# Optimization experiments

Measured on AMD Instinct MI355X. Metric: run time of the kernel, lower is better.

Reference implementation:

```python
import jax, jax.numpy as jnp
import numpy as np

N = 100000      # num nodes
E = 1600000     # num edges (avg degree 16)
D_IN = 64
D_OUT = 32
NEG_SLOPE = 0.01  # torch LeakyReLU default


def setup_inputs() -> dict:
    key = jax.random.key(0)
    k1, k2, k3, k4 = jax.random.split(key, 4)
    x = jax.random.normal(k1, (N, D_IN), dtype=jnp.float32)
    edge_index = jax.random.randint(k2, (2, E), 0, N, dtype=jnp.int32)
    # GCNConv linear weights (glorot-ish init) and biases
    W1 = jax.random.normal(k3, (D_IN, D_IN), dtype=jnp.float32) / np.float32(np.sqrt(D_IN))
    b1 = jnp.zeros((D_IN,), dtype=jnp.float32)
    W2 = jax.random.normal(k4, (D_IN, D_OUT), dtype=jnp.float32) / np.float32(np.sqrt(D_IN))
    b2 = jnp.zeros((D_OUT,), dtype=jnp.float32)
    return {"x": x, "edge_index": edge_index, "W1": W1, "b1": b1, "W2": W2, "b2": b2}


def reference(x, edge_index, W1, b1, W2, b2):
    # PyG GCNConv default: add self-loops, symmetric normalization D^-1/2 (A+I) D^-1/2
    loops = jnp.arange(N, dtype=edge_index.dtype)
    src = jnp.concatenate([edge_index[0], loops])  # [E+N]
    dst = jnp.concatenate([edge_index[1], loops])  # [E+N]
    deg = jax.ops.segment_sum(jnp.ones(src.shape[0], jnp.float32), dst, num_segments=N)
    dinv = jax.lax.rsqrt(deg)  # deg >= 1 due to self-loops
    norm = dinv[src] * dinv[dst]  # [E+N]

    def gcn_conv(h, W, b):
        h = h @ W                          # [N, d_out]
        msg = h[src] * norm[:, None]       # gather + normalize  [E+N, d_out]
        return jax.ops.segment_sum(msg, dst, num_segments=N) + b  # scatter-add

    h = gcn_conv(x, W1, b1)
    h = jnp.where(h > 0, h, NEG_SLOPE * h)  # LeakyReLU
    return gcn_conv(h, W2, b2)
```

## Files before the change

kernel.cpp:

```cpp
#include <hip/hip_runtime.h>

#define N_NODES 100000
#define N_EDGES 1600000
#define DIN 64
#define DOUT 32
#define NEG_SLOPE 0.01f
#define NBUCK 196
#define CAP 12288
#define CH 4096
#define NB1 ((N_EDGES + CH - 1) / CH)

__device__ inline unsigned short f2bf(float f) {
    unsigned int u = __float_as_uint(f);
    unsigned int r = (u + 0x7fffu + ((u >> 16) & 1u)) >> 16;
    return (unsigned short)r;
}
__device__ inline float bflo(unsigned int p) { return __uint_as_float(p << 16); }
__device__ inline float bfhi(unsigned int p) { return __uint_as_float(p & 0xffff0000u); }
#define NTL(p) __builtin_nontemporal_load(p)

__device__ inline void addpack4(float* a, uint4 r) {
    a[0] += bflo(r.x); a[1] += bfhi(r.x);
    a[2] += bflo(r.y); a[3] += bfhi(r.y);
    a[4] += bflo(r.z); a[5] += bfhi(r.z);
    a[6] += bflo(r.w); a[7] += bfhi(r.w);
}
__device__ inline void addpack2(float* a, uint2 r) {
    a[0] += bflo(r.x); a[1] += bfhi(r.x);
    a[2] += bflo(r.y); a[3] += bfhi(r.y);
}

__global__ __launch_bounds__(256) void binpass1_kernel(const int* __restrict__ src,
                                                       const int* __restrict__ dst,
                                                       int* __restrict__ bucketfill,
                                                       unsigned int* __restrict__ staging2) {
    __shared__ int histw[4][NBUCK];
    __shared__ int base[NBUCK];
    __shared__ int tot[NBUCK];
    __shared__ int gbase[NBUCK];
    __shared__ int scanbuf[256];
    __shared__ unsigned int sorted[CH];
    int tid = threadIdx.x;
    int w = tid >> 6;
    int b = blockIdx.x;
    for (int t = tid; t < 4 * NBUCK; t += 256) ((int*)histw)[t] = 0;
    __syncthreads();

    int e0 = b * CH + tid;
    int bk[16];
    int rk[16];
    unsigned int pay[16];
#pragma unroll
    for (int i = 0; i < 16; ++i) {
        int e = e0 + i * 256;
        if (e < N_EDGES) {
            int d = NTL(&dst[e]);
            int s = NTL(&src[e]);
            bk[i] = d >> 9;
            pay[i] = (unsigned int)s | ((unsigned int)(d & 511) << 17);
            rk[i] = atomicAdd(&histw[w][bk[i]], 1);
        } else {
            bk[i] = -1;
        }
    }
    __syncthreads();
    int v = 0;
    if (tid < NBUCK) {
        int h0 = histw[0][tid], h1 = histw[1][tid], h2 = histw[2][tid], h3 = histw[3][tid];
        histw[0][tid] = 0;
        histw[1][tid] = h0;
        histw[2][tid] = h0 + h1;
        histw[3][tid] = h0 + h1 + h2;
        v = h0 + h1 + h2 + h3;
        tot[tid] = v;
    }
    scanbuf[tid] = (tid < NBUCK) ? v : 0;
    __syncthreads();
    for (int off = 1; off < 256; off <<= 1) {
        int a = scanbuf[tid];
        int add = (tid >= off) ? scanbuf[tid - off] : 0;
        __syncthreads();
        scanbuf[tid] = a + add;
        __syncthreads();
    }
    if (tid < NBUCK) {
        base[tid] = scanbuf[tid] - v;
        gbase[tid] = v ? atomicAdd(&bucketfill[tid], v) : 0;
    }
    __syncthreads();
#pragma unroll
    for (int i = 0; i < 16; ++i) {
        if (bk[i] >= 0) sorted[base[bk[i]] + histw[w][bk[i]] + rk[i]] = pay[i];
    }
    __syncthreads();
    int wv = tid >> 6, ln = tid & 63;
    for (int k = wv; k < NBUCK; k += 4) {
        int h = tot[k];
        int b0 = base[k];
        int g0 = gbase[k];
        unsigned int* dp = staging2 + (size_t)k * CAP;
        for (int i = ln; i < h; i += 64)
            if (g0 + i < CAP) dp[g0 + i] = sorted[b0 + i];
    }
}

__global__ __launch_bounds__(1024) void binpass2_kernel(const unsigned int* __restrict__ staging2,
                                                        const int* __restrict__ bucketfill,
                                                        int* __restrict__ rowptr,
                                                        float* __restrict__ dinv,
                                                        int* __restrict__ colsrc) {
    __shared__ unsigned int coll[CAP];
    __shared__ int hist[512];
    __shared__ int posl[512];
    __shared__ int sh[512];
    __shared__ int red[4];
    int k = blockIdx.x;
    int tid = threadIdx.x;
    int base_node = k << 9;
    int nn = min(512, N_NODES - base_node);
    int len = min(bucketfill[k], CAP);

    if (tid < 256) {
        int v = (tid < k) ? bucketfill[tid] : 0;
#pragma unroll
        for (int off = 32; off; off >>= 1) v += __shfl_down(v, off);
        if ((tid & 63) == 0) red[tid >> 6] = v;
    }
    if (tid < 512) hist[tid] = 0;
    __syncthreads();
    int bbase = red[0] + red[1] + red[2] + red[3];
    const unsigned int* stg = staging2 + (size_t)k * CAP;

    for (int i = tid; i < len; i += 1024) coll[i] = NTL(&stg[i]);
    __syncthreads();
    for (int i = tid; i < len; i += 1024) atomicAdd(&hist[coll[i] >> 17], 1);
    __syncthreads();

    int v = 0;
    if (tid < 512) { v = hist[tid]; sh[tid] = v; }
    __syncthreads();
    for (int off = 1; off < 512; off <<= 1) {
        int a = 0, add = 0;
        if (tid < 512) { a = sh[tid]; add = (tid >= off) ? sh[tid - off] : 0; }
        __syncthreads();
        if (tid < 512) sh[tid] = a + add;
        __syncthreads();
    }
    if (tid < 512) {
        int excl = sh[tid] - v;
        posl[tid] = bbase + excl;
        if (tid < nn) {
            rowptr[base_node + tid] = bbase + excl;
            dinv[base_node + tid] = rsqrtf((float)(v + 1));
        }
    }
    if (k == NBUCK - 1 && tid == 0) rowptr[N_NODES] = N_EDGES;
    __syncthreads();
    for (int i = tid; i < len; i += 1024) {
        unsigned int pay = coll[i];
        int idx = atomicAdd(&posl[pay >> 17], 1);
        colsrc[idx] = (int)(pay & 0x1FFFFu);
    }
}

__global__ __launch_bounds__(256) void gemm_k64_n64_kernel(const float* __restrict__ X,
                                                           const float* __restrict__ W,
                                                           const float* __restrict__ dinv,
                                                           unsigned short* __restrict__ Hn) {
    __shared__ float Ws[64 * 64];
    __shared__ float Xs[64][65];
    int tid = threadIdx.x;
    int row0 = blockIdx.x * 64;
    {
        const float4* Wv = (const float4*)W;
        float4* Wsv = (float4*)Ws;
#pragma unroll
        for (int i = 0; i < 4; ++i) Wsv[tid + 256 * i] = Wv[tid + 256 * i];
    }
#pragma unroll
    for (int i = 0; i < 4; ++i) {
        int s = tid + i * 256;
        int r = s >> 4, c = (s & 15) * 4;
        int gr = row0 + r;
        float4 xv = (gr < N_NODES) ? *(const float4*)(X + (size_t)gr * 64 + c)
                                   : make_float4(0.f, 0.f, 0.f, 0.f);
        Xs[r][c] = xv.x; Xs[r][c + 1] = xv.y; Xs[r][c + 2] = xv.z; Xs[r][c + 3] = xv.w;
    }
    __syncthreads();

    int c4 = (tid & 15) * 4;
    int r4 = (tid >> 4) * 4;
    float a0[4] = {}, a1[4] = {}, a2[4] = {}, a3[4] = {};
#pragma unroll 8
    for (int k = 0; k < 64; ++k) {
        float4 w = *(const float4*)&Ws[(k << 6) + c4];
        float x0 = Xs[r4][k], x1 = Xs[r4 + 1][k], x2 = Xs[r4 + 2][k], x3 = Xs[r4 + 3][k];
        a0[0] += x0 * w.x; a0[1] += x0 * w.y; a0[2] += x0 * w.z; a0[3] += x0 * w.w;
        a1[0] += x1 * w.x; a1[1] += x1 * w.y; a1[2] += x1 * w.z; a1[3] += x1 * w.w;
        a2[0] += x2 * w.x; a2[1] += x2 * w.y; a2[2] += x2 * w.z; a2[3] += x2 * w.w;
        a3[0] += x3 * w.x; a3[1] += x3 * w.y; a3[2] += x3 * w.z; a3[3] += x3 * w.w;
    }
    float* accs[4] = {a0, a1, a2, a3};
#pragma unroll
    for (int r = 0; r < 4; ++r) {
        int gr = row0 + r4 + r;
        if (gr < N_NODES) {
            float dv = dinv[gr];
            float* a = accs[r];
            unsigned int lo = (unsigned int)f2bf(a[0] * dv) | ((unsigned int)f2bf(a[1] * dv) << 16);
            unsigned int hi = (unsigned int)f2bf(a[2] * dv) | ((unsigned int)f2bf(a[3] * dv) << 16);
            *(uint2*)(Hn + (size_t)gr * 64 + c4) = make_uint2(lo, hi);
        }
    }
}

__global__ __launch_bounds__(256) void gather64_fused_kernel(
    const unsigned short* __restrict__ Hn, const int* __restrict__ rowptr,
    const int* __restrict__ colsrc, const float* __restrict__ dinv,
    const float* __restrict__ bias, const float* __restrict__ W2,
    unsigned short* __restrict__ h2n) {
    __shared__ float R[32][65];
    __shared__ float W2s[64][32];
    int tid = threadIdx.x;
    {
        const float4* Wv = (const float4*)W2;
        float4* Wsv = (float4*)W2s;
#pragma unroll
        for (int i = 0; i < 2; ++i) Wsv[tid + 256 * i] = Wv[tid + 256 * i];
    }

    int lane = tid & 63;
    int w = tid >> 6;
    int g = lane >> 3, sl = lane & 7, gb = g << 3;
    int nodeLocal = w * 8 + g;
    int v = blockIdx.x * 32 + nodeLocal;
    int beg = rowptr[v], end = rowptr[v + 1];

    float acc[8], ac2[8];
#pragma unroll
    for (int i = 0; i < 8; ++i) { acc[i] = 0.f; ac2[i] = 0.f; }
    {
        uint4 rw = ((const uint4*)(Hn + (size_t)v * 64))[sl];
        addpack4(acc, rw);
    }
    int t0 = beg;
    for (; t0 + 8 <= end; t0 += 8) {
        int sv = colsrc[t0 + sl];
        uint4 r[8];
#pragma unroll
        for (int t = 0; t < 8; ++t) {
            int s = __shfl(sv, gb + t);
            r[t] = ((const uint4*)(Hn + (size_t)s * 64))[sl];
        }
#pragma unroll
        for (int t = 0; t < 8; t += 2) {
            addpack4(acc, r[t]);
            addpack4(ac2, r[t + 1]);
        }
    }
    if (t0 < end) {
        int sv = (t0 + sl < end) ? colsrc[t0 + sl] : 0;
        int cnt = end - t0;
        int t = 0;
        for (; t + 2 <= cnt; t += 2) {
            int s0 = __shfl(sv, gb + t);
            int s1 = __shfl(sv, gb + t + 1);
            uint4 r0 = ((const uint4*)(Hn + (size_t)s0 * 64))[sl];
            uint4 r1 = ((const uint4*)(Hn + (size_t)s1 * 64))[sl];
            addpack4(acc, r0);
            addpack4(ac2, r1);
        }
        if (t < cnt) {
            int s0 = __shfl(sv, gb + t);
            uint4 r0 = ((const uint4*)(Hn + (size_t)s0 * 64))[sl];
            addpack4(acc, r0);
        }
    }
    float dv = dinv[v];
    float4 b0 = ((const float4*)(bias + sl * 8))[0];
    float4 b1v = ((const float4*)(bias + sl * 8))[1];
    float o[8];
    o[0] = (acc[0] + ac2[0]) * dv + b0.x;  o[1] = (acc[1] + ac2[1]) * dv + b0.y;
    o[2] = (acc[2] + ac2[2]) * dv + b0.z;  o[3] = (acc[3] + ac2[3]) * dv + b0.w;
    o[4] = (acc[4] + ac2[4]) * dv + b1v.x; o[5] = (acc[5] + ac2[5]) * dv + b1v.y;
    o[6] = (acc[6] + ac2[6]) * dv + b1v.z; o[7] = (acc[7] + ac2[7]) * dv + b1v.w;
#pragma unroll
    for (int i = 0; i < 8; ++i) o[i] = o[i] > 0.f ? o[i] : NEG_SLOPE * o[i];
    *(float4*)&R[nodeLocal][sl * 8] = make_float4(o[0], o[1], o[2], o[3]);
    *(float4*)&R[nodeLocal][sl * 8 + 4] = make_float4(o[4], o[5], o[6], o[7]);
    __syncthreads();

    int row = tid >> 3;
    int c4 = (tid & 7) * 4;
    float a[4] = {};
#pragma unroll 8
    for (int k = 0; k < 64; ++k) {
        float x = R[row][k];
        float4 wv = *(const float4*)&W2s[k][c4];
        a[0] += x * wv.x; a[1] += x * wv.y; a[2] += x * wv.z; a[3] += x * wv.w;
    }
    int gv = blockIdx.x * 32 + row;
    float dv2 = dinv[gv];
    unsigned int lo = (unsigned int)f2bf(a[0] * dv2) | ((unsigned int)f2bf(a[1] * dv2) << 16);
    unsigned int hi = (unsigned int)f2bf(a[2] * dv2) | ((unsigned int)f2bf(a[3] * dv2) << 16);
    *(uint2*)(h2n + (size_t)gv * 32 + c4) = make_uint2(lo, hi);
}

__global__ __launch_bounds__(256) void gather32_kernel(
    const unsigned short* __restrict__ Hn, const int* __restrict__ rowptr,
    const int* __restrict__ colsrc, const float* __restrict__ dinv,
    const float* __restrict__ bias, float* __restrict__ out) {
    int gwid = (blockIdx.x * blockDim.x + threadIdx.x) >> 6;
    int lane = threadIdx.x & 63;
    int g = lane >> 3, sl = lane & 7, gb = g << 3;
    int v = gwid * 8 + g;
    if (v >= N_NODES) return;
    int beg = rowptr[v], end = rowptr[v + 1];

    float acc[4], ac2[4];
#pragma unroll
    for (int i = 0; i < 4; ++i) { acc[i] = 0.f; ac2[i] = 0.f; }
    {
        uint2 rw = ((const uint2*)(Hn + (size_t)v * 32))[sl];
        addpack2(acc, rw);
    }
    int t0 = beg;
    for (; t0 + 8 <= end; t0 += 8) {
        int sv = colsrc[t0 + sl];
        uint2 r[8];
#pragma unroll
        for (int t = 0; t < 8; ++t) {
            int s = __shfl(sv, gb + t);
            r[t] = ((const uint2*)(Hn + (size_t)s * 32))[sl];
        }
#pragma unroll
        for (int t = 0; t < 8; t += 2) {
            addpack2(acc, r[t]);
            addpack2(ac2, r[t + 1]);
        }
    }
    if (t0 < end) {
        int sv = (t0 + sl < end) ? colsrc[t0 + sl] : 0;
        int cnt = end - t0;
        int t = 0;
        for (; t + 2 <= cnt; t += 2) {
            int s0 = __shfl(sv, gb + t);
            int s1 = __shfl(sv, gb + t + 1);
            uint2 r0 = ((const uint2*)(Hn + (size_t)s0 * 32))[sl];
            uint2 r1 = ((const uint2*)(Hn + (size_t)s1 * 32))[sl];
            addpack2(acc, r0);
            addpack2(ac2, r1);
        }
        if (t < cnt) {
            int s0 = __shfl(sv, gb + t);
            uint2 r0 = ((const uint2*)(Hn + (size_t)s0 * 32))[sl];
            addpack2(acc, r0);
        }
    }
    float dv = dinv[v];
    float4 bb = ((const float4*)bias)[sl];
    float o0 = (acc[0] + ac2[0]) * dv + bb.x;
    float o1 = (acc[1] + ac2[1]) * dv + bb.y;
    float o2 = (acc[2] + ac2[2]) * dv + bb.z;
    float o3 = (acc[3] + ac2[3]) * dv + bb.w;
    *(float4*)(out + (size_t)v * 32 + sl * 4) = make_float4(o0, o1, o2, o3);
}

extern "C" void kernel_launch(void* const* d_in, const int* in_sizes, int n_in,
                              void* d_out, int out_size, void* d_ws, size_t ws_size,
                              hipStream_t stream) {
    const float* x = (const float*)d_in[0];
    const int* ei = (const int*)d_in[1];
    const float* W1 = (const float*)d_in[2];
    const float* b1 = (const float*)d_in[3];
    const float* W2 = (const float*)d_in[4];
    const float* b2 = (const float*)d_in[5];
    float* out = (float*)d_out;

    const int* src = ei;
    const int* dst = ei + N_EDGES;

    char* p = (char*)d_ws;
    auto alloc = [&](size_t bytes) { char* r = p; p += (bytes + 255) & ~(size_t)255; return r; };
    float* dinv = (float*)alloc(N_NODES * 4);
    int* rowptr = (int*)alloc((N_NODES + 1) * 4);
    int* bucketfill = (int*)alloc(NBUCK * 4);
    int* colsrc = (int*)alloc((size_t)N_EDGES * 4);
    unsigned short* h1n = (unsigned short*)alloc((size_t)N_NODES * DIN * 2);
    unsigned short* h2n = (unsigned short*)alloc((size_t)N_NODES * DOUT * 2);
    unsigned int* staging2 = (unsigned int*)alloc((size_t)NBUCK * CAP * 4);

    hipMemsetAsync(bucketfill, 0, NBUCK * sizeof(int), stream);
    binpass1_kernel<<<NB1, 256, 0, stream>>>(src, dst, bucketfill, staging2);
    binpass2_kernel<<<NBUCK, 1024, 0, stream>>>(staging2, bucketfill, rowptr, dinv, colsrc);

    gemm_k64_n64_kernel<<<(N_NODES + 63) / 64, 256, 0, stream>>>(x, W1, dinv, h1n);

    gather64_fused_kernel<<<N_NODES / 32, 256, 0, stream>>>(
        h1n, rowptr, colsrc, dinv, b1, W2, h2n);

    gather32_kernel<<<(N_NODES / 8 * 64) / 256, 256, 0, stream>>>(
        h2n, rowptr, colsrc, dinv, b2, out);
}
```

Baseline: 128.5 us.

## Sort nodes by degree within buckets to balance gather warp workloads

Binning now also computes a per-512-node permutation that groups nodes by in-degree (capped at 63) via a counting sort in shared memory. Both gather kernels process nodes in this permuted order, so the 8 nodes sharing a wavefront have similar edge counts and lanes idle less on divergent loop trip counts. The cost is extra shared atomics and a scan in binpass2, one more indirection per node, and less locality in output and self-row accesses.

```diff
diff --git a/kernel.cpp b/kernel.cpp
--- a/kernel.cpp
+++ b/kernel.cpp
@@ -108,12 +108,15 @@
                                                         const int* __restrict__ bucketfill,
                                                         int* __restrict__ rowptr,
                                                         float* __restrict__ dinv,
-                                                        int* __restrict__ colsrc) {
+                                                        int* __restrict__ colsrc,
+                                                        int* __restrict__ perm) {
     __shared__ unsigned int coll[CAP];
     __shared__ int hist[512];
     __shared__ int posl[512];
     __shared__ int sh[512];
     __shared__ int red[4];
+    __shared__ int chist[64];
+    __shared__ int cbase[64];
     int k = blockIdx.x;
     int tid = threadIdx.x;
     int base_node = k << 9;
@@ -127,6 +130,7 @@
         if ((tid & 63) == 0) red[tid >> 6] = v;
     }
     if (tid < 512) hist[tid] = 0;
+    if (tid >= 512 && tid < 576) chist[tid - 512] = 0;
     __syncthreads();
     int bbase = red[0] + red[1] + red[2] + red[3];
     const unsigned int* stg = staging2 + (size_t)k * CAP;
@@ -146,16 +150,31 @@
         if (tid < 512) sh[tid] = a + add;
         __syncthreads();
     }
+    int crank = 0, ccls = 0;
     if (tid < 512) {
         int excl = sh[tid] - v;
         posl[tid] = bbase + excl;
         if (tid < nn) {
             rowptr[base_node + tid] = bbase + excl;
             dinv[base_node + tid] = rsqrtf((float)(v + 1));
+            ccls = min(v, 63);
+            crank = atomicAdd(&chist[ccls], 1);
         }
     }
     if (k == NBUCK - 1 && tid == 0) rowptr[N_NODES] = N_EDGES;
     __syncthreads();
+    if (tid < 64) {
+        int c = chist[tid];
+        int x = c;
+#pragma unroll
+        for (int off = 1; off < 64; off <<= 1) {
+            int n = __shfl_up(x, off);
+            if ((tid & 63) >= off) x += n;
+        }
+        cbase[tid] = x - c;
+    }
+    __syncthreads();
+    if (tid < nn) perm[base_node + cbase[ccls] + crank] = base_node + tid;
     for (int i = tid; i < len; i += 1024) {
         unsigned int pay = coll[i];
         int idx = atomicAdd(&posl[pay >> 17], 1);
@@ -218,9 +237,10 @@
     const unsigned short* __restrict__ Hn, const int* __restrict__ rowptr,
     const int* __restrict__ colsrc, const float* __restrict__ dinv,
     const float* __restrict__ bias, const float* __restrict__ W2,
-    unsigned short* __restrict__ h2n) {
+    const int* __restrict__ perm, unsigned short* __restrict__ h2n) {
     __shared__ float R[32][65];
     __shared__ float W2s[64][32];
+    __shared__ int vperm[32];
     int tid = threadIdx.x;
     {
         const float4* Wv = (const float4*)W2;
@@ -228,12 +248,14 @@
 #pragma unroll
         for (int i = 0; i < 2; ++i) Wsv[tid + 256 * i] = Wv[tid + 256 * i];
     }
+    if (tid < 32) vperm[tid] = perm[blockIdx.x * 32 + tid];
+    __syncthreads();
 
     int lane = tid & 63;
     int w = tid >> 6;
     int g = lane >> 3, sl = lane & 7, gb = g << 3;
     int nodeLocal = w * 8 + g;
-    int v = blockIdx.x * 32 + nodeLocal;
+    int v = vperm[nodeLocal];
     int beg = rowptr[v], end = rowptr[v + 1];
 
     float acc[8], ac2[8];
@@ -299,7 +321,7 @@
         float4 wv = *(const float4*)&W2s[k][c4];
         a[0] += x * wv.x; a[1] += x * wv.y; a[2] += x * wv.z; a[3] += x * wv.w;
     }
-    int gv = blockIdx.x * 32 + row;
+    int gv = vperm[row];
     float dv2 = dinv[gv];
     unsigned int lo = (unsigned int)f2bf(a[0] * dv2) | ((unsigned int)f2bf(a[1] * dv2) << 16);
     unsigned int hi = (unsigned int)f2bf(a[2] * dv2) | ((unsigned int)f2bf(a[3] * dv2) << 16);
@@ -309,12 +331,14 @@
 __global__ __launch_bounds__(256) void gather32_kernel(
     const unsigned short* __restrict__ Hn, const int* __restrict__ rowptr,
     const int* __restrict__ colsrc, const float* __restrict__ dinv,
-    const float* __restrict__ bias, float* __restrict__ out) {
+    const float* __restrict__ bias, const int* __restrict__ perm,
+    float* __restrict__ out) {
     int gwid = (blockIdx.x * blockDim.x + threadIdx.x) >> 6;
     int lane = threadIdx.x & 63;
     int g = lane >> 3, sl = lane & 7, gb = g << 3;
-    int v = gwid * 8 + g;
-    if (v >= N_NODES) return;
+    int vi = gwid * 8 + g;
+    if (vi >= N_NODES) return;
+    int v = perm[vi];
     int beg = rowptr[v], end = rowptr[v + 1];
 
     float acc[4], ac2[4];
@@ -385,6 +409,7 @@
     float* dinv = (float*)alloc(N_NODES * 4);
     int* rowptr = (int*)alloc((N_NODES + 1) * 4);
     int* bucketfill = (int*)alloc(NBUCK * 4);
+    int* perm = (int*)alloc(N_NODES * 4);
     int* colsrc = (int*)alloc((size_t)N_EDGES * 4);
     unsigned short* h1n = (unsigned short*)alloc((size_t)N_NODES * DIN * 2);
     unsigned short* h2n = (unsigned short*)alloc((size_t)N_NODES * DOUT * 2);
@@ -392,13 +417,13 @@
 
     hipMemsetAsync(bucketfill, 0, NBUCK * sizeof(int), stream);
     binpass1_kernel<<<NB1, 256, 0, stream>>>(src, dst, bucketfill, staging2);
-    binpass2_kernel<<<NBUCK, 1024, 0, stream>>>(staging2, bucketfill, rowptr, dinv, colsrc);
+    binpass2_kernel<<<NBUCK, 1024, 0, stream>>>(staging2, bucketfill, rowptr, dinv, colsrc, perm);
 
     gemm_k64_n64_kernel<<<(N_NODES + 63) / 64, 256, 0, stream>>>(x, W1, dinv, h1n);
 
     gather64_fused_kernel<<<N_NODES / 32, 256, 0, stream>>>(
-        h1n, rowptr, colsrc, dinv, b1, W2, h2n);
+        h1n, rowptr, colsrc, dinv, b1, W2, perm, h2n);
 
     gather32_kernel<<<(N_NODES / 8 * 64) / 256, 256, 0, stream>>>(
-        h2n, rowptr, colsrc, dinv, b2, out);
-}
+        h2n, rowptr, colsrc, dinv, b2, perm, out);
+}
```

Result: slower. 140.8 us (+9.5%).
